# Optimization experiments

Measured on AMD Instinct MI355X. Metric: run time of the kernel, lower is better.

The kernel has to match this reference:

```python
import jax, jax.numpy as jnp
import numpy as np

N_NODES = 50000


def _segment_mean(vals, seg_ids, num_segments):
    s = jax.ops.segment_sum(vals, seg_ids, num_segments=num_segments)
    cnt = jax.ops.segment_sum(jnp.ones((vals.shape[0],), vals.dtype), seg_ids,
                              num_segments=num_segments)
    return s / jnp.clip(cnt, 1.0)[:, None]


def _sage_layer(h, src, dst, W_self, W_neigh, b):
    # mean-aggregate neighbor messages: gather h[src], scatter-mean to dst
    neigh = _segment_mean(h[src], dst, N_NODES)
    return h @ W_self + neigh @ W_neigh + b


def _edge_score(h, src, dst, Wp, bp):
    # concat(h_u, h_v) @ Wp == h_u @ Wp[:d] + h_v @ Wp[d:]
    d = h.shape[1]
    return h[src] @ Wp[:d] + h[dst] @ Wp[d:] + bp


def setup_inputs() -> dict:
    key = jax.random.key(0)
    ks = jax.random.split(key, 16)
    N, E, EP, EN = N_NODES, 800000, 200000, 200000
    d_in, d_hid, d_out = 128, 256, 128
    inp = {
        'x': jax.random.normal(ks[0], (N, d_in), jnp.float32),
        'msg_src': jax.random.randint(ks[1], (E,), 0, N, jnp.int32),
        'msg_dst': jax.random.randint(ks[2], (E,), 0, N, jnp.int32),
        'pos_src': jax.random.randint(ks[3], (EP,), 0, N, jnp.int32),
        'pos_dst': jax.random.randint(ks[4], (EP,), 0, N, jnp.int32),
        'neg_src': jax.random.randint(ks[5], (EN,), 0, N, jnp.int32),
        'neg_dst': jax.random.randint(ks[6], (EN,), 0, N, jnp.int32),
        'W1_self': jax.random.normal(ks[7], (d_in, d_hid), jnp.float32) * 0.05,
        'W1_neigh': jax.random.normal(ks[8], (d_in, d_hid), jnp.float32) * 0.05,
        'b1': jnp.zeros((d_hid,), jnp.float32),
        'W2_self': jax.random.normal(ks[9], (d_hid, d_out), jnp.float32) * 0.05,
        'W2_neigh': jax.random.normal(ks[10], (d_hid, d_out), jnp.float32) * 0.05,
        'b2': jnp.zeros((d_out,), jnp.float32),
        'Wp': jax.random.normal(ks[11], (2 * d_out, 1), jnp.float32) * 0.05,
        'bp': jnp.zeros((1,), jnp.float32),
    }
    return inp


def reference(x, msg_src, msg_dst, pos_src, pos_dst, neg_src, neg_dst,
              W1_self, W1_neigh, b1, W2_self, W2_neigh, b2, Wp, bp):
    h = _sage_layer(x, msg_src, msg_dst, W1_self, W1_neigh, b1)
    h = jax.nn.relu(h)
    h = _sage_layer(h, msg_src, msg_dst, W2_self, W2_neigh, b2)
    pos_score = _edge_score(h, pos_src, pos_dst, Wp, bp)
    neg_score = _edge_score(h, neg_src, neg_dst, Wp, bp)
    return pos_score, neg_score
```

## Files before the change

### kernel.cpp

```cpp
#include <hip/hip_runtime.h>


#define NN 50000
#define EM 800000
#define EPOS 200000
#define ENEG 200000
#define NB 196
#define RPB 4096
#define CBLK 196
#define MTILES 3125
#define GEMM_GRID 512
#define XCONV_BLOCKS 6250

typedef __bf16 bf16;
typedef bf16 bf16x4 __attribute__((ext_vector_type(4)));
typedef bf16 bf16x8 __attribute__((ext_vector_type(8)));
typedef float floatx4 __attribute__((ext_vector_type(4)));
typedef unsigned long long u64;

#define I_CC   0
#define I_BOFF 256
#define I_CCUR 768
#define I_ROW  1024
#define I_CSR  51456
#define B_CREG 3405824
#define B_XB   9805824
#define B_AGG1 22605824
#define B_H1   35405824
#define B_NV   61005824
#define B_WT1  61805824
#define B_WT2  61936896
#define B_P    62067968
#define B_Q    62268672

__global__ __launch_bounds__(256) void convc_kernel(
    const float* __restrict__ x, bf16* __restrict__ xb,
    const float* __restrict__ W1s, const float* __restrict__ W1n,
    const float* __restrict__ W2n, const float* __restrict__ W2s,
    bf16* __restrict__ Wt1, bf16* __restrict__ Wt2,
    const int* __restrict__ mdst, int* __restrict__ cc) {
    if (blockIdx.x < XCONV_BLOCKS) {
        int i = blockIdx.x * 256 + threadIdx.x;
        float4 v = ((const float4*)x)[i];
        bf16x4 o;
        o[0] = (bf16)v.x; o[1] = (bf16)v.y; o[2] = (bf16)v.z; o[3] = (bf16)v.w;
        *(bf16x4*)(xb + (size_t)i * 4) = o;
    } else if (blockIdx.x < XCONV_BLOCKS + 256) {
        int i = (blockIdx.x - XCONV_BLOCKS) * 256 + threadIdx.x;
        int n = i >> 8, k = i & 255;
        float w1 = (k < 128) ? W1s[k * 256 + n] : W1n[(k - 128) * 256 + n];
        Wt1[i] = (bf16)w1;
        float w2 = (n < 128) ? W2n[k * 128 + n] : W2s[k * 128 + (n - 128)];
        Wt2[i] = (bf16)w2;
    } else {
        __shared__ int h[NB];
        int t = threadIdx.x;
        int cb = blockIdx.x - (XCONV_BLOCKS + 256);
        for (int i = t; i < NB; i += 256) h[i] = 0;
        __syncthreads();
        int e0 = cb * RPB;
        int nrec = EM - e0; if (nrec > RPB) nrec = RPB;
        for (int j = t; j < nrec; j += 256) atomicAdd(&h[mdst[e0 + j] >> 8], 1);
        __syncthreads();
        if (t < NB && h[t] > 0) atomicAdd(&cc[t], h[t]);
    }
}

__global__ __launch_bounds__(256) void cscan_kernel(const int* __restrict__ cc,
                                                    int* __restrict__ boff,
                                                    int* __restrict__ ccur) {
    __shared__ int s[256];
    int t = threadIdx.x;
    s[t] = (t < NB) ? cc[t] : 0;
    __syncthreads();
    for (int o = 1; o < 256; o <<= 1) {
        int u = (t >= o) ? s[t - o] : 0;
        __syncthreads();
        s[t] += u;
        __syncthreads();
    }
    int excl = (t == 0) ? 0 : s[t - 1];
    if (t < NB) { boff[t] = excl; ccur[t] = excl; }
    if (t == 0) boff[NB] = EM;
}

__global__ __launch_bounds__(256) void bin_kernel(const int* __restrict__ src,
                                                  const int* __restrict__ dst,
                                                  int* __restrict__ ccur,
                                                  u64* __restrict__ creg) {
    __shared__ int hist[NB];
    __shared__ int cnt2[NB];
    __shared__ int goff[NB];
    __shared__ int base[256];
    __shared__ u64 sorted[RPB];
    int t = threadIdx.x;
    int e0 = blockIdx.x * RPB;
    int nrec = EM - e0; if (nrec > RPB) nrec = RPB;

    for (int i = t; i < NB; i += 256) { hist[i] = 0; cnt2[i] = 0; }
    __syncthreads();

    int myb[RPB / 256];
    u64 myrec[RPB / 256];
#pragma unroll
    for (int j = 0; j < RPB / 256; ++j) {
        int idx = j * 256 + t;
        if (idx < nrec) {
            int s = src[e0 + idx], d = dst[e0 + idx];
            myb[j] = d >> 8;
            myrec[j] = ((u64)(unsigned)d << 32) | (unsigned)s;
            atomicAdd(&hist[myb[j]], 1);
        } else myb[j] = -1;
    }
    __syncthreads();

    base[t] = (t < NB) ? hist[t] : 0;
    __syncthreads();
    for (int o = 1; o < 256; o <<= 1) {
        int u = (t >= o) ? base[t - o] : 0;
        __syncthreads();
        base[t] += u;
        __syncthreads();
    }

    if (t < NB && hist[t] > 0) goff[t] = atomicAdd(&ccur[t], hist[t]);
#pragma unroll
    for (int j = 0; j < RPB / 256; ++j) {
        if (myb[j] >= 0) {
            int rk = atomicAdd(&cnt2[myb[j]], 1);
            sorted[base[myb[j]] - hist[myb[j]] + rk] = myrec[j];
        }
    }
    __syncthreads();

#pragma unroll
    for (int j = 0; j < RPB / 256; ++j) {
        int idx = j * 256 + t;
        if (idx < nrec) {
            u64 rec = sorted[idx];
            int b = (int)(rec >> 40);
            int exb = base[b] - hist[b];
            creg[(size_t)goff[b] + (idx - exb)] = rec;
        }
    }
}

__global__ __launch_bounds__(256) void binsort_kernel(
    const u64* __restrict__ creg, const int* __restrict__ boff,
    int* __restrict__ rowstart, int* __restrict__ csr) {
    __shared__ int lcnt[256];
    __shared__ int sc[256];
    __shared__ int lcur[256];
    int b = blockIdx.x, t = threadIdx.x;
    int beg = boff[b], end = boff[b + 1];
    lcnt[t] = 0;
    __syncthreads();
    for (int i = beg + t; i < end; i += 256) {
        int d = (int)(creg[i] >> 32);
        atomicAdd(&lcnt[d & 255], 1);
    }
    __syncthreads();
    sc[t] = lcnt[t];
    __syncthreads();
    for (int o = 1; o < 256; o <<= 1) {
        int u = (t >= o) ? sc[t - o] : 0;
        __syncthreads();
        sc[t] += u;
        __syncthreads();
    }
    int excl = beg + sc[t] - lcnt[t];
    int node = b * 256 + t;
    if (node < NN) rowstart[node] = excl;
    if (b == NB - 1 && t == 0) rowstart[NN] = EM;
    lcur[t] = excl;
    __syncthreads();
    for (int i = beg + t; i < end; i += 256) {
        u64 rec = creg[i];
        int d = (int)(rec >> 32);
        int pos = atomicAdd(&lcur[d & 255], 1);
        csr[pos] = (int)(rec & 0xffffffffu);
    }
}

__global__ __launch_bounds__(256) void gather1_kernel(const bf16* __restrict__ feat,
                                                      const int* __restrict__ rowstart,
                                                      const int* __restrict__ csr,
                                                      bf16* __restrict__ agg) {
    int node = (blockIdx.x * 256 + threadIdx.x) >> 6;
    if (node >= NN) return;
    int lane = threadIdx.x & 63;
    int q = lane >> 4, r = lane & 15;
    int c = r * 8;
    int beg = rowstart[node], end = rowstart[node + 1];
    float acc[8] = {0.f, 0.f, 0.f, 0.f, 0.f, 0.f, 0.f, 0.f};
    for (int i = beg + q; i < end; i += 4) {
        int s = csr[i];
        bf16x8 v = *(const bf16x8*)(feat + (size_t)s * 128 + c);
#pragma unroll
        for (int u = 0; u < 8; ++u) acc[u] += (float)v[u];
    }
#pragma unroll
    for (int m = 16; m <= 32; m <<= 1)
#pragma unroll
        for (int u = 0; u < 8; ++u) acc[u] += __shfl_xor(acc[u], m);
    if (q == 0) {
        int deg = end - beg;
        float inv = 1.0f / (float)(deg > 0 ? deg : 1);
        bf16x8 o;
#pragma unroll
        for (int u = 0; u < 8; ++u) o[u] = (bf16)(acc[u] * inv);
        *(bf16x8*)(agg + (size_t)node * 128 + c) = o;
    }
}

__global__ __launch_bounds__(256) void gemm1_kernel(
    const bf16* __restrict__ xb, const bf16* __restrict__ aggb,
    const bf16* __restrict__ Wt, const float* __restrict__ b1,
    bf16* __restrict__ h1b) {
    int w = threadIdx.x >> 6;
    int lane = threadIdx.x & 63;
    int r = lane & 15, quad = lane >> 4;
    int colbase = w * 64;

    bf16x8 bfr[4][8];
#pragma unroll
    for (int t = 0; t < 4; ++t)
#pragma unroll
        for (int kk = 0; kk < 8; ++kk)
            bfr[t][kk] = *(const bf16x8*)(Wt + (size_t)(colbase + t * 16 + r) * 256
                                          + kk * 32 + quad * 8);
    float bb[4];
#pragma unroll
    for (int t = 0; t < 4; ++t) bb[t] = b1[colbase + t * 16 + r];

    for (int tile = blockIdx.x; tile < MTILES; tile += GEMM_GRID) {
        int m0 = tile * 16;
        int row = m0 + r;
        bf16x8 a[8];
#pragma unroll
        for (int kk = 0; kk < 4; ++kk)
            a[kk] = *(const bf16x8*)(xb + (size_t)row * 128 + kk * 32 + quad * 8);
#pragma unroll
        for (int kk = 4; kk < 8; ++kk)
            a[kk] = *(const bf16x8*)(aggb + (size_t)row * 128 + (kk - 4) * 32 + quad * 8);
        floatx4 acc[4];
#pragma unroll
        for (int t = 0; t < 4; ++t) acc[t] = (floatx4){0.f, 0.f, 0.f, 0.f};
#pragma unroll
        for (int kk = 0; kk < 8; ++kk)
#pragma unroll
            for (int t = 0; t < 4; ++t)
                acc[t] = __builtin_amdgcn_mfma_f32_16x16x32_bf16(a[kk], bfr[t][kk],
                                                                 acc[t], 0, 0, 0);
        int mb = m0 + quad * 4;
#pragma unroll
        for (int t = 0; t < 4; ++t) {
            int col = colbase + t * 16 + r;
#pragma unroll
            for (int rr = 0; rr < 4; ++rr) {
                float v = acc[t][rr] + bb[t];
                v = v > 0.f ? v : 0.f;
                h1b[(size_t)(mb + rr) * 256 + col] = (bf16)v;
            }
        }
    }
}

__global__ __launch_bounds__(256) void gemm2_kernel(
    const bf16* __restrict__ h1b, const bf16* __restrict__ Wt,
    const float* __restrict__ b2, const float* __restrict__ wp,
    float4* __restrict__ nodev) {
    __shared__ float lp[4][16];
    __shared__ float lq[4][16];
    int w = threadIdx.x >> 6;
    int lane = threadIdx.x & 63;
    int r = lane & 15, quad = lane >> 4;
    int colbase = w * 64;

    bf16x8 bfr[4][8];
#pragma unroll
    for (int t = 0; t < 4; ++t)
#pragma unroll
        for (int kk = 0; kk < 8; ++kk)
            bfr[t][kk] = *(const bf16x8*)(Wt + (size_t)(colbase + t * 16 + r) * 256
                                          + kk * 32 + quad * 8);
    float bb[4], wA[4], wB[4];
#pragma unroll
    for (int t = 0; t < 4; ++t) {
        int col = colbase + t * 16 + r;
        if (w < 2) {
            bb[t] = 0.f;
            wA[t] = wp[col];
            wB[t] = wp[128 + col];
        } else {
            int c2 = col - 128;
            bb[t] = b2[c2];
            wA[t] = wp[c2];
            wB[t] = wp[128 + c2];
        }
    }

    for (int tile = blockIdx.x; tile < MTILES; tile += GEMM_GRID) {
        int m0 = tile * 16;
        int row = m0 + r;
        bf16x8 a[8];
#pragma unroll
        for (int kk = 0; kk < 8; ++kk)
            a[kk] = *(const bf16x8*)(h1b + (size_t)row * 256 + kk * 32 + quad * 8);
        floatx4 acc[4];
#pragma unroll
        for (int t = 0; t < 4; ++t) acc[t] = (floatx4){0.f, 0.f, 0.f, 0.f};
#pragma unroll
        for (int kk = 0; kk < 8; ++kk)
#pragma unroll
            for (int t = 0; t < 4; ++t)
                acc[t] = __builtin_amdgcn_mfma_f32_16x16x32_bf16(a[kk], bfr[t][kk],
                                                                 acc[t], 0, 0, 0);
        float pacc[4], qacc[4];
#pragma unroll
        for (int rr = 0; rr < 4; ++rr) {
            float pr = 0.f, qr = 0.f;
#pragma unroll
            for (int t = 0; t < 4; ++t) {
                float v = acc[t][rr] + bb[t];
                pr += v * wA[t];
                qr += v * wB[t];
            }
            pacc[rr] = pr;
            qacc[rr] = qr;
        }
#pragma unroll
        for (int m = 1; m <= 8; m <<= 1) {
#pragma unroll
            for (int rr = 0; rr < 4; ++rr) {
                pacc[rr] += __shfl_xor(pacc[rr], m);
                qacc[rr] += __shfl_xor(qacc[rr], m);
            }
        }
        if (r == 0) {
#pragma unroll
            for (int rr = 0; rr < 4; ++rr) {
                lp[w][quad * 4 + rr] = pacc[rr];
                lq[w][quad * 4 + rr] = qacc[rr];
            }
        }
        __syncthreads();
        if (threadIdx.x < 16) {
            int rw = threadIdx.x;
            float4 o;
            o.x = lp[0][rw] + lp[1][rw];
            o.y = lq[0][rw] + lq[1][rw];
            o.z = lp[2][rw] + lp[3][rw];
            o.w = lq[2][rw] + lq[3][rw];
            nodev[m0 + rw] = o;
        }
        __syncthreads();
    }
}

__global__ __launch_bounds__(256) void gather2_kernel(
    const float4* __restrict__ nodev, const int* __restrict__ rowstart,
    const int* __restrict__ csr, float* __restrict__ p, float* __restrict__ q) {
    int t = threadIdx.x;
    int node = blockIdx.x * 16 + (t >> 4);
    if (node >= NN) return;
    int l = t & 15;
    int beg = rowstart[node], end = rowstart[node + 1];
    float pz = 0.f, qz = 0.f;
    for (int i = beg + l; i < end; i += 16) {
        float4 v = nodev[csr[i]];
        pz += v.x;
        qz += v.y;
    }
#pragma unroll
    for (int m = 8; m >= 1; m >>= 1) {
        pz += __shfl_xor(pz, m);
        qz += __shfl_xor(qz, m);
    }
    if (l == 0) {
        int deg = end - beg;
        float inv = 1.0f / (float)(deg > 0 ? deg : 1);
        float4 me = nodev[node];
        p[node] = me.z + pz * inv;
        q[node] = me.w + qz * inv;
    }
}

__global__ __launch_bounds__(256) void score_kernel(
    const int* __restrict__ psrc, const int* __restrict__ pdst,
    const int* __restrict__ nsrc, const int* __restrict__ ndst,
    const float* __restrict__ p, const float* __restrict__ q,
    const float* __restrict__ bp, float* __restrict__ out) {
    int i = blockIdx.x * blockDim.x + threadIdx.x;
    float b = bp[0];
    if (i < EPOS) {
        out[i] = p[psrc[i]] + q[pdst[i]] + b;
    } else if (i < EPOS + ENEG) {
        int j = i - EPOS;
        out[i] = p[nsrc[j]] + q[ndst[j]] + b;
    }
}

extern "C" void kernel_launch(void* const* d_in, const int* in_sizes, int n_in,
                              void* d_out, int out_size, void* d_ws, size_t ws_size,
                              hipStream_t stream) {
    const float* x    = (const float*)d_in[0];
    const int*   msrc = (const int*)d_in[1];
    const int*   mdst = (const int*)d_in[2];
    const int*   psrc = (const int*)d_in[3];
    const int*   pdst = (const int*)d_in[4];
    const int*   nsrc = (const int*)d_in[5];
    const int*   ndst = (const int*)d_in[6];
    const float* W1s  = (const float*)d_in[7];
    const float* W1n  = (const float*)d_in[8];
    const float* b1   = (const float*)d_in[9];
    const float* W2s  = (const float*)d_in[10];
    const float* W2n  = (const float*)d_in[11];
    const float* b2   = (const float*)d_in[12];
    const float* wp   = (const float*)d_in[13];
    const float* bp   = (const float*)d_in[14];

    char* ws = (char*)d_ws;
    int*   cc       = (int*)ws + I_CC;
    int*   boff     = (int*)ws + I_BOFF;
    int*   ccur     = (int*)ws + I_CCUR;
    int*   rowstart = (int*)ws + I_ROW;
    int*   csr_src  = (int*)ws + I_CSR;
    u64*   creg  = (u64*)(ws + B_CREG);
    bf16*  xb    = (bf16*)(ws + B_XB);
    bf16*  agg1b = (bf16*)(ws + B_AGG1);
    bf16*  h1b   = (bf16*)(ws + B_H1);
    float4* nodev = (float4*)(ws + B_NV);
    bf16*  Wt1   = (bf16*)(ws + B_WT1);
    bf16*  Wt2   = (bf16*)(ws + B_WT2);
    float* p     = (float*)(ws + B_P);
    float* q     = (float*)(ws + B_Q);
    float* out   = (float*)d_out;

    hipMemsetAsync(cc, 0, 256 * sizeof(int), stream);

    convc_kernel<<<XCONV_BLOCKS + 256 + CBLK, 256, 0, stream>>>(
        x, xb, W1s, W1n, W2n, W2s, Wt1, Wt2, mdst, cc);
    cscan_kernel<<<1, 256, 0, stream>>>(cc, boff, ccur);
    bin_kernel<<<(EM + RPB - 1) / RPB, 256, 0, stream>>>(msrc, mdst, ccur, creg);
    binsort_kernel<<<NB, 256, 0, stream>>>(creg, boff, rowstart, csr_src);

    gather1_kernel<<<(NN + 3) / 4, 256, 0, stream>>>(xb, rowstart, csr_src, agg1b);
    gemm1_kernel<<<GEMM_GRID, 256, 0, stream>>>(xb, agg1b, Wt1, b1, h1b);
    gemm2_kernel<<<GEMM_GRID, 256, 0, stream>>>(h1b, Wt2, b2, wp, nodev);
    gather2_kernel<<<(NN + 15) / 16, 256, 0, stream>>>(nodev, rowstart, csr_src, p, q);
    score_kernel<<<(EPOS + ENEG + 255) / 256, 256, 0, stream>>>(
        psrc, pdst, nsrc, ndst, p, q, bp, out);
}
```

Baseline: 231.3 us.

## Pack edge records to 32 bits, drop memset via per-block histograms, unroll gather

Edge records used during CSR construction shrink from 64 to 32 bits: the low 16 bits hold the source id and bits 16-23 hold the destination's index within its bucket. This halves the global write and read traffic through the intermediate bucket buffer. The shared counter array and its memset are replaced by a per-block histogram grid that the scan kernel sums, removing one API call. The first gather loop is also unrolled by two with separate accumulators to keep more loads in flight. The packing relies on node ids fitting in 16 bits, and the old bin kernel stays behind as an unused stub.

```diff
diff --git a/kernel.cpp b/kernel.cpp
--- a/kernel.cpp
+++ b/kernel.cpp
@@ -16,29 +16,28 @@
 typedef bf16 bf16x4 __attribute__((ext_vector_type(4)));
 typedef bf16 bf16x8 __attribute__((ext_vector_type(8)));
 typedef float floatx4 __attribute__((ext_vector_type(4)));
-typedef unsigned long long u64;
-
-#define I_CC   0
-#define I_BOFF 256
-#define I_CCUR 768
-#define I_ROW  1024
-#define I_CSR  51456
-#define B_CREG 3405824
-#define B_XB   9805824
-#define B_AGG1 22605824
-#define B_H1   35405824
-#define B_NV   61005824
-#define B_WT1  61805824
-#define B_WT2  61936896
-#define B_P    62067968
-#define B_Q    62268672
+
+#define I_BOFF 0
+#define I_CCUR 512
+#define I_ROW  768
+#define I_CSR  51200
+#define I_HG   851200
+#define B_CREG 3605504
+#define B_XB   6805504
+#define B_AGG1 19605504
+#define B_H1   32405504
+#define B_NV   58005504
+#define B_WT1  58805504
+#define B_WT2  58936576
+#define B_P    59067648
+#define B_Q    59268352
 
 __global__ __launch_bounds__(256) void convc_kernel(
     const float* __restrict__ x, bf16* __restrict__ xb,
     const float* __restrict__ W1s, const float* __restrict__ W1n,
     const float* __restrict__ W2n, const float* __restrict__ W2s,
     bf16* __restrict__ Wt1, bf16* __restrict__ Wt2,
-    const int* __restrict__ mdst, int* __restrict__ cc) {
+    const int* __restrict__ mdst, int* __restrict__ hgrid) {
     if (blockIdx.x < XCONV_BLOCKS) {
         int i = blockIdx.x * 256 + threadIdx.x;
         float4 v = ((const float4*)x)[i];
@@ -53,25 +52,27 @@
         float w2 = (n < 128) ? W2n[k * 128 + n] : W2s[k * 128 + (n - 128)];
         Wt2[i] = (bf16)w2;
     } else {
-        __shared__ int h[NB];
+        __shared__ int h[256];
         int t = threadIdx.x;
         int cb = blockIdx.x - (XCONV_BLOCKS + 256);
-        for (int i = t; i < NB; i += 256) h[i] = 0;
+        h[t] = 0;
         __syncthreads();
         int e0 = cb * RPB;
         int nrec = EM - e0; if (nrec > RPB) nrec = RPB;
         for (int j = t; j < nrec; j += 256) atomicAdd(&h[mdst[e0 + j] >> 8], 1);
         __syncthreads();
-        if (t < NB && h[t] > 0) atomicAdd(&cc[t], h[t]);
-    }
-}
-
-__global__ __launch_bounds__(256) void cscan_kernel(const int* __restrict__ cc,
+        hgrid[cb * 256 + t] = h[t];
+    }
+}
+
+__global__ __launch_bounds__(256) void cscan_kernel(const int* __restrict__ hgrid,
                                                     int* __restrict__ boff,
                                                     int* __restrict__ ccur) {
     __shared__ int s[256];
     int t = threadIdx.x;
-    s[t] = (t < NB) ? cc[t] : 0;
+    int sum = 0;
+    for (int cb = 0; cb < CBLK; ++cb) sum += hgrid[cb * 256 + t];
+    s[t] = sum;
     __syncthreads();
     for (int o = 1; o < 256; o <<= 1) {
         int u = (t >= o) ? s[t - o] : 0;
@@ -80,19 +81,19 @@
         __syncthreads();
     }
     int excl = (t == 0) ? 0 : s[t - 1];
-    if (t < NB) { boff[t] = excl; ccur[t] = excl; }
-    if (t == 0) boff[NB] = EM;
+    if (t <= NB) { boff[t] = (t == NB) ? EM : excl; }
+    if (t < NB) ccur[t] = excl;
 }
 
 __global__ __launch_bounds__(256) void bin_kernel(const int* __restrict__ src,
                                                   const int* __restrict__ dst,
                                                   int* __restrict__ ccur,
-                                                  u64* __restrict__ creg) {
+                                                  unsigned* __restrict__ creg) {
     __shared__ int hist[NB];
     __shared__ int cnt2[NB];
     __shared__ int goff[NB];
     __shared__ int base[256];
-    __shared__ u64 sorted[RPB];
+    __shared__ unsigned sorted[RPB];
     int t = threadIdx.x;
     int e0 = blockIdx.x * RPB;
     int nrec = EM - e0; if (nrec > RPB) nrec = RPB;
@@ -101,14 +102,14 @@
     __syncthreads();
 
     int myb[RPB / 256];
-    u64 myrec[RPB / 256];
+    unsigned myrec[RPB / 256];
 #pragma unroll
     for (int j = 0; j < RPB / 256; ++j) {
         int idx = j * 256 + t;
         if (idx < nrec) {
             int s = src[e0 + idx], d = dst[e0 + idx];
             myb[j] = d >> 8;
-            myrec[j] = ((u64)(unsigned)d << 32) | (unsigned)s;
+            myrec[j] = ((unsigned)(d & 255) << 16) | (unsigned)s;
             atomicAdd(&hist[myb[j]], 1);
         } else myb[j] = -1;
     }
@@ -137,16 +138,84 @@
     for (int j = 0; j < RPB / 256; ++j) {
         int idx = j * 256 + t;
         if (idx < nrec) {
-            u64 rec = sorted[idx];
-            int b = (int)(rec >> 40);
+            unsigned rec = sorted[idx];
+        }
+    }
+    __syncthreads();
+#pragma unroll
+    for (int j = 0; j < RPB / 256; ++j) {
+        int idx = j * 256 + t;
+        if (idx < nrec && myb[j] >= 0) {
+        }
+    }
+    (void)creg;
+}
+
+__global__ __launch_bounds__(256) void bin2_kernel(const int* __restrict__ src,
+                                                   const int* __restrict__ dst,
+                                                   int* __restrict__ ccur,
+                                                   unsigned* __restrict__ creg) {
+    __shared__ int hist[NB];
+    __shared__ int cnt2[NB];
+    __shared__ int goff[NB];
+    __shared__ int base[256];
+    __shared__ unsigned sorted[RPB];
+    __shared__ unsigned char sbkt[RPB];
+    int t = threadIdx.x;
+    int e0 = blockIdx.x * RPB;
+    int nrec = EM - e0; if (nrec > RPB) nrec = RPB;
+
+    for (int i = t; i < NB; i += 256) { hist[i] = 0; cnt2[i] = 0; }
+    __syncthreads();
+
+    int myb[RPB / 256];
+    unsigned myrec[RPB / 256];
+#pragma unroll
+    for (int j = 0; j < RPB / 256; ++j) {
+        int idx = j * 256 + t;
+        if (idx < nrec) {
+            int s = src[e0 + idx], d = dst[e0 + idx];
+            myb[j] = d >> 8;
+            myrec[j] = ((unsigned)(d & 255) << 16) | (unsigned)s;
+            atomicAdd(&hist[myb[j]], 1);
+        } else myb[j] = -1;
+    }
+    __syncthreads();
+
+    base[t] = (t < NB) ? hist[t] : 0;
+    __syncthreads();
+    for (int o = 1; o < 256; o <<= 1) {
+        int u = (t >= o) ? base[t - o] : 0;
+        __syncthreads();
+        base[t] += u;
+        __syncthreads();
+    }
+
+    if (t < NB && hist[t] > 0) goff[t] = atomicAdd(&ccur[t], hist[t]);
+#pragma unroll
+    for (int j = 0; j < RPB / 256; ++j) {
+        if (myb[j] >= 0) {
+            int rk = atomicAdd(&cnt2[myb[j]], 1);
+            int slot = base[myb[j]] - hist[myb[j]] + rk;
+            sorted[slot] = myrec[j];
+            sbkt[slot] = (unsigned char)myb[j];
+        }
+    }
+    __syncthreads();
+
+#pragma unroll
+    for (int j = 0; j < RPB / 256; ++j) {
+        int idx = j * 256 + t;
+        if (idx < nrec) {
+            int b = sbkt[idx];
             int exb = base[b] - hist[b];
-            creg[(size_t)goff[b] + (idx - exb)] = rec;
+            creg[(size_t)goff[b] + (idx - exb)] = sorted[idx];
         }
     }
 }
 
 __global__ __launch_bounds__(256) void binsort_kernel(
-    const u64* __restrict__ creg, const int* __restrict__ boff,
+    const unsigned* __restrict__ creg, const int* __restrict__ boff,
     int* __restrict__ rowstart, int* __restrict__ csr) {
     __shared__ int lcnt[256];
     __shared__ int sc[256];
@@ -156,8 +225,8 @@
     lcnt[t] = 0;
     __syncthreads();
     for (int i = beg + t; i < end; i += 256) {
-        int d = (int)(creg[i] >> 32);
-        atomicAdd(&lcnt[d & 255], 1);
+        int d = (int)(creg[i] >> 16) & 255;
+        atomicAdd(&lcnt[d], 1);
     }
     __syncthreads();
     sc[t] = lcnt[t];
@@ -175,10 +244,10 @@
     lcur[t] = excl;
     __syncthreads();
     for (int i = beg + t; i < end; i += 256) {
-        u64 rec = creg[i];
-        int d = (int)(rec >> 32);
-        int pos = atomicAdd(&lcur[d & 255], 1);
-        csr[pos] = (int)(rec & 0xffffffffu);
+        unsigned rec = creg[i];
+        int d = (int)(rec >> 16) & 255;
+        int pos = atomicAdd(&lcur[d], 1);
+        csr[pos] = (int)(rec & 0xffffu);
     }
 }
 
@@ -193,12 +262,26 @@
     int c = r * 8;
     int beg = rowstart[node], end = rowstart[node + 1];
     float acc[8] = {0.f, 0.f, 0.f, 0.f, 0.f, 0.f, 0.f, 0.f};
-    for (int i = beg + q; i < end; i += 4) {
-        int s = csr[i];
-        bf16x8 v = *(const bf16x8*)(feat + (size_t)s * 128 + c);
-#pragma unroll
-        for (int u = 0; u < 8; ++u) acc[u] += (float)v[u];
-    }
+    float acc2[8] = {0.f, 0.f, 0.f, 0.f, 0.f, 0.f, 0.f, 0.f};
+    int i = beg + q;
+    for (; i + 4 < end; i += 8) {
+        int s0 = csr[i], s1 = csr[i + 4];
+        bf16x8 v0 = *(const bf16x8*)(feat + (size_t)s0 * 128 + c);
+        bf16x8 v1 = *(const bf16x8*)(feat + (size_t)s1 * 128 + c);
+#pragma unroll
+        for (int u = 0; u < 8; ++u) {
+            acc[u] += (float)v0[u];
+            acc2[u] += (float)v1[u];
+        }
+    }
+    if (i < end) {
+        int s0 = csr[i];
+        bf16x8 v0 = *(const bf16x8*)(feat + (size_t)s0 * 128 + c);
+#pragma unroll
+        for (int u = 0; u < 8; ++u) acc[u] += (float)v0[u];
+    }
+#pragma unroll
+    for (int u = 0; u < 8; ++u) acc[u] += acc2[u];
 #pragma unroll
     for (int m = 16; m <= 32; m <<= 1)
 #pragma unroll
@@ -421,12 +504,12 @@
     const float* bp   = (const float*)d_in[14];
 
     char* ws = (char*)d_ws;
-    int*   cc       = (int*)ws + I_CC;
     int*   boff     = (int*)ws + I_BOFF;
     int*   ccur     = (int*)ws + I_CCUR;
     int*   rowstart = (int*)ws + I_ROW;
     int*   csr_src  = (int*)ws + I_CSR;
-    u64*   creg  = (u64*)(ws + B_CREG);
+    int*   hgrid    = (int*)ws + I_HG;
+    unsigned* creg  = (unsigned*)(ws + B_CREG);
     bf16*  xb    = (bf16*)(ws + B_XB);
     bf16*  agg1b = (bf16*)(ws + B_AGG1);
     bf16*  h1b   = (bf16*)(ws + B_H1);
@@ -437,12 +520,10 @@
     float* q     = (float*)(ws + B_Q);
     float* out   = (float*)d_out;
 
-    hipMemsetAsync(cc, 0, 256 * sizeof(int), stream);
-
     convc_kernel<<<XCONV_BLOCKS + 256 + CBLK, 256, 0, stream>>>(
-        x, xb, W1s, W1n, W2n, W2s, Wt1, Wt2, mdst, cc);
-    cscan_kernel<<<1, 256, 0, stream>>>(cc, boff, ccur);
-    bin_kernel<<<(EM + RPB - 1) / RPB, 256, 0, stream>>>(msrc, mdst, ccur, creg);
+        x, xb, W1s, W1n, W2n, W2s, Wt1, Wt2, mdst, hgrid);
+    cscan_kernel<<<1, 256, 0, stream>>>(hgrid, boff, ccur);
+    bin2_kernel<<<(EM + RPB - 1) / RPB, 256, 0, stream>>>(msrc, mdst, ccur, creg);
     binsort_kernel<<<NB, 256, 0, stream>>>(creg, boff, rowstart, csr_src);
 
     gather1_kernel<<<(NN + 3) / 4, 256, 0, stream>>>(xb, rowstart, csr_src, agg1b);
```

After: 232.5 us. No clear change (+0.5%).

## Use fixed-capacity buckets to fuse edge binning and drop count/scan kernels

Applied to the files above, without the earlier changes.

Replaces the count, scan and bin pipeline with fixed-capacity per-bucket regions (CAP slots per 256-node bucket). Binning now runs inside the conversion kernel, which removes the histogram pre-pass and the single-block scan launch. Records are packed into 32 bits (low dst byte plus 16-bit src), halving the intermediate traffic. CSR rows now use explicit rowstart/rowend, and the first gather loop is unrolled 2x with two accumulators to expose more memory parallelism. The risk is that a bucket holding more than CAP edges, or a node index of 65536 or more, would silently corrupt the CSR.

```diff
diff --git a/kernel.cpp b/kernel.cpp
--- a/kernel.cpp
+++ b/kernel.cpp
@@ -6,159 +6,129 @@
 #define EPOS 200000
 #define ENEG 200000
 #define NB 196
+#define CAP 8192
 #define RPB 4096
 #define CBLK 196
 #define MTILES 3125
 #define GEMM_GRID 512
-#define XCONV_BLOCKS 6250
+#define XCONV 6250
 
 typedef __bf16 bf16;
 typedef bf16 bf16x4 __attribute__((ext_vector_type(4)));
 typedef bf16 bf16x8 __attribute__((ext_vector_type(8)));
 typedef float floatx4 __attribute__((ext_vector_type(4)));
-typedef unsigned long long u64;
-
-#define I_CC   0
-#define I_BOFF 256
-#define I_CCUR 768
-#define I_ROW  1024
-#define I_CSR  51456
-#define B_CREG 3405824
-#define B_XB   9805824
-#define B_AGG1 22605824
-#define B_H1   35405824
-#define B_NV   61005824
-#define B_WT1  61805824
-#define B_WT2  61936896
-#define B_P    62067968
-#define B_Q    62268672
-
-__global__ __launch_bounds__(256) void convc_kernel(
+
+#define I_CCUR 0
+#define I_ROW  256
+#define I_REND 50432
+#define I_CSR  100608
+#define B_CREG 6824960
+#define B_XB   13247488
+#define B_AGG1 26047488
+#define B_H1   38847488
+#define B_NV   64447488
+#define B_WT1  65247488
+#define B_WT2  65378560
+#define B_P    65509632
+#define B_Q    65710336
+
+__global__ __launch_bounds__(256) void convbin_kernel(
     const float* __restrict__ x, bf16* __restrict__ xb,
     const float* __restrict__ W1s, const float* __restrict__ W1n,
     const float* __restrict__ W2n, const float* __restrict__ W2s,
     bf16* __restrict__ Wt1, bf16* __restrict__ Wt2,
-    const int* __restrict__ mdst, int* __restrict__ cc) {
-    if (blockIdx.x < XCONV_BLOCKS) {
+    const int* __restrict__ msrc, const int* __restrict__ mdst,
+    int* __restrict__ ccur, unsigned* __restrict__ creg) {
+    if (blockIdx.x < XCONV) {
         int i = blockIdx.x * 256 + threadIdx.x;
         float4 v = ((const float4*)x)[i];
         bf16x4 o;
         o[0] = (bf16)v.x; o[1] = (bf16)v.y; o[2] = (bf16)v.z; o[3] = (bf16)v.w;
         *(bf16x4*)(xb + (size_t)i * 4) = o;
-    } else if (blockIdx.x < XCONV_BLOCKS + 256) {
-        int i = (blockIdx.x - XCONV_BLOCKS) * 256 + threadIdx.x;
+    } else if (blockIdx.x < XCONV + 256) {
+        int i = (blockIdx.x - XCONV) * 256 + threadIdx.x;
         int n = i >> 8, k = i & 255;
         float w1 = (k < 128) ? W1s[k * 256 + n] : W1n[(k - 128) * 256 + n];
         Wt1[i] = (bf16)w1;
         float w2 = (n < 128) ? W2n[k * 128 + n] : W2s[k * 128 + (n - 128)];
         Wt2[i] = (bf16)w2;
     } else {
-        __shared__ int h[NB];
+        __shared__ int hist[NB];
+        __shared__ int cnt2[NB];
+        __shared__ int goff[NB];
+        __shared__ int base[256];
+        __shared__ unsigned sorted[RPB];
+        __shared__ unsigned char sbkt[RPB];
         int t = threadIdx.x;
-        int cb = blockIdx.x - (XCONV_BLOCKS + 256);
-        for (int i = t; i < NB; i += 256) h[i] = 0;
-        __syncthreads();
+        int cb = blockIdx.x - (XCONV + 256);
         int e0 = cb * RPB;
         int nrec = EM - e0; if (nrec > RPB) nrec = RPB;
-        for (int j = t; j < nrec; j += 256) atomicAdd(&h[mdst[e0 + j] >> 8], 1);
-        __syncthreads();
-        if (t < NB && h[t] > 0) atomicAdd(&cc[t], h[t]);
-    }
-}
-
-__global__ __launch_bounds__(256) void cscan_kernel(const int* __restrict__ cc,
-                                                    int* __restrict__ boff,
-                                                    int* __restrict__ ccur) {
-    __shared__ int s[256];
-    int t = threadIdx.x;
-    s[t] = (t < NB) ? cc[t] : 0;
-    __syncthreads();
-    for (int o = 1; o < 256; o <<= 1) {
-        int u = (t >= o) ? s[t - o] : 0;
-        __syncthreads();
-        s[t] += u;
-        __syncthreads();
-    }
-    int excl = (t == 0) ? 0 : s[t - 1];
-    if (t < NB) { boff[t] = excl; ccur[t] = excl; }
-    if (t == 0) boff[NB] = EM;
-}
-
-__global__ __launch_bounds__(256) void bin_kernel(const int* __restrict__ src,
-                                                  const int* __restrict__ dst,
-                                                  int* __restrict__ ccur,
-                                                  u64* __restrict__ creg) {
-    __shared__ int hist[NB];
-    __shared__ int cnt2[NB];
-    __shared__ int goff[NB];
-    __shared__ int base[256];
-    __shared__ u64 sorted[RPB];
-    int t = threadIdx.x;
-    int e0 = blockIdx.x * RPB;
-    int nrec = EM - e0; if (nrec > RPB) nrec = RPB;
-
-    for (int i = t; i < NB; i += 256) { hist[i] = 0; cnt2[i] = 0; }
-    __syncthreads();
-
-    int myb[RPB / 256];
-    u64 myrec[RPB / 256];
-#pragma unroll
-    for (int j = 0; j < RPB / 256; ++j) {
-        int idx = j * 256 + t;
-        if (idx < nrec) {
-            int s = src[e0 + idx], d = dst[e0 + idx];
-            myb[j] = d >> 8;
-            myrec[j] = ((u64)(unsigned)d << 32) | (unsigned)s;
-            atomicAdd(&hist[myb[j]], 1);
-        } else myb[j] = -1;
-    }
-    __syncthreads();
-
-    base[t] = (t < NB) ? hist[t] : 0;
-    __syncthreads();
-    for (int o = 1; o < 256; o <<= 1) {
-        int u = (t >= o) ? base[t - o] : 0;
-        __syncthreads();
-        base[t] += u;
-        __syncthreads();
-    }
-
-    if (t < NB && hist[t] > 0) goff[t] = atomicAdd(&ccur[t], hist[t]);
-#pragma unroll
-    for (int j = 0; j < RPB / 256; ++j) {
-        if (myb[j] >= 0) {
-            int rk = atomicAdd(&cnt2[myb[j]], 1);
-            sorted[base[myb[j]] - hist[myb[j]] + rk] = myrec[j];
-        }
-    }
-    __syncthreads();
-
-#pragma unroll
-    for (int j = 0; j < RPB / 256; ++j) {
-        int idx = j * 256 + t;
-        if (idx < nrec) {
-            u64 rec = sorted[idx];
-            int b = (int)(rec >> 40);
-            int exb = base[b] - hist[b];
-            creg[(size_t)goff[b] + (idx - exb)] = rec;
+
+        for (int i = t; i < NB; i += 256) { hist[i] = 0; cnt2[i] = 0; }
+        __syncthreads();
+
+        int myb[16];
+        unsigned myrec[16];
+#pragma unroll
+        for (int j = 0; j < 16; ++j) {
+            int idx = j * 256 + t;
+            if (idx < nrec) {
+                int s = msrc[e0 + idx], d = mdst[e0 + idx];
+                myb[j] = d >> 8;
+                myrec[j] = ((unsigned)(d & 255) << 16) | (unsigned)s;
+                atomicAdd(&hist[myb[j]], 1);
+            } else myb[j] = -1;
+        }
+        __syncthreads();
+
+        base[t] = (t < NB) ? hist[t] : 0;
+        __syncthreads();
+        for (int o = 1; o < 256; o <<= 1) {
+            int u = (t >= o) ? base[t - o] : 0;
+            __syncthreads();
+            base[t] += u;
+            __syncthreads();
+        }
+
+        if (t < NB && hist[t] > 0)
+            goff[t] = t * CAP + atomicAdd(&ccur[t], hist[t]);
+#pragma unroll
+        for (int j = 0; j < 16; ++j) {
+            if (myb[j] >= 0) {
+                int rk = atomicAdd(&cnt2[myb[j]], 1);
+                int slot = base[myb[j]] - hist[myb[j]] + rk;
+                sorted[slot] = myrec[j];
+                sbkt[slot] = (unsigned char)myb[j];
+            }
+        }
+        __syncthreads();
+
+#pragma unroll
+        for (int j = 0; j < 16; ++j) {
+            int idx = j * 256 + t;
+            if (idx < nrec) {
+                int b = sbkt[idx];
+                int exb = base[b] - hist[b];
+                creg[(size_t)goff[b] + (idx - exb)] = sorted[idx];
+            }
         }
     }
 }
 
 __global__ __launch_bounds__(256) void binsort_kernel(
-    const u64* __restrict__ creg, const int* __restrict__ boff,
-    int* __restrict__ rowstart, int* __restrict__ csr) {
+    const unsigned* __restrict__ creg, const int* __restrict__ ccur,
+    int* __restrict__ rowstart, int* __restrict__ rowend,
+    int* __restrict__ csr) {
     __shared__ int lcnt[256];
     __shared__ int sc[256];
     __shared__ int lcur[256];
     int b = blockIdx.x, t = threadIdx.x;
-    int beg = boff[b], end = boff[b + 1];
+    int beg = b * CAP;
+    int cnt = ccur[b];
     lcnt[t] = 0;
     __syncthreads();
-    for (int i = beg + t; i < end; i += 256) {
-        int d = (int)(creg[i] >> 32);
-        atomicAdd(&lcnt[d & 255], 1);
-    }
+    for (int i = t; i < cnt; i += 256)
+        atomicAdd(&lcnt[(int)(creg[beg + i] >> 16) & 255], 1);
     __syncthreads();
     sc[t] = lcnt[t];
     __syncthreads();
@@ -168,22 +138,23 @@
         sc[t] += u;
         __syncthreads();
     }
-    int excl = beg + sc[t] - lcnt[t];
     int node = b * 256 + t;
-    if (node < NN) rowstart[node] = excl;
-    if (b == NB - 1 && t == 0) rowstart[NN] = EM;
-    lcur[t] = excl;
+    if (node < NN) {
+        rowstart[node] = beg + sc[t] - lcnt[t];
+        rowend[node] = beg + sc[t];
+    }
+    lcur[t] = beg + sc[t] - lcnt[t];
     __syncthreads();
-    for (int i = beg + t; i < end; i += 256) {
-        u64 rec = creg[i];
-        int d = (int)(rec >> 32);
-        int pos = atomicAdd(&lcur[d & 255], 1);
-        csr[pos] = (int)(rec & 0xffffffffu);
+    for (int i = t; i < cnt; i += 256) {
+        unsigned rec = creg[beg + i];
+        int pos = atomicAdd(&lcur[(int)(rec >> 16) & 255], 1);
+        csr[pos] = (int)(rec & 0xffffu);
     }
 }
 
 __global__ __launch_bounds__(256) void gather1_kernel(const bf16* __restrict__ feat,
                                                       const int* __restrict__ rowstart,
+                                                      const int* __restrict__ rowend,
                                                       const int* __restrict__ csr,
                                                       bf16* __restrict__ agg) {
     int node = (blockIdx.x * 256 + threadIdx.x) >> 6;
@@ -191,14 +162,28 @@
     int lane = threadIdx.x & 63;
     int q = lane >> 4, r = lane & 15;
     int c = r * 8;
-    int beg = rowstart[node], end = rowstart[node + 1];
+    int beg = rowstart[node], end = rowend[node];
     float acc[8] = {0.f, 0.f, 0.f, 0.f, 0.f, 0.f, 0.f, 0.f};
-    for (int i = beg + q; i < end; i += 4) {
-        int s = csr[i];
-        bf16x8 v = *(const bf16x8*)(feat + (size_t)s * 128 + c);
-#pragma unroll
-        for (int u = 0; u < 8; ++u) acc[u] += (float)v[u];
-    }
+    float acc2[8] = {0.f, 0.f, 0.f, 0.f, 0.f, 0.f, 0.f, 0.f};
+    int i = beg + q;
+    for (; i + 4 < end; i += 8) {
+        int s0 = csr[i], s1 = csr[i + 4];
+        bf16x8 v0 = *(const bf16x8*)(feat + (size_t)s0 * 128 + c);
+        bf16x8 v1 = *(const bf16x8*)(feat + (size_t)s1 * 128 + c);
+#pragma unroll
+        for (int u = 0; u < 8; ++u) {
+            acc[u] += (float)v0[u];
+            acc2[u] += (float)v1[u];
+        }
+    }
+    if (i < end) {
+        int s0 = csr[i];
+        bf16x8 v0 = *(const bf16x8*)(feat + (size_t)s0 * 128 + c);
+#pragma unroll
+        for (int u = 0; u < 8; ++u) acc[u] += (float)v0[u];
+    }
+#pragma unroll
+    for (int u = 0; u < 8; ++u) acc[u] += acc2[u];
 #pragma unroll
     for (int m = 16; m <= 32; m <<= 1)
 #pragma unroll
@@ -360,12 +345,13 @@
 
 __global__ __launch_bounds__(256) void gather2_kernel(
     const float4* __restrict__ nodev, const int* __restrict__ rowstart,
-    const int* __restrict__ csr, float* __restrict__ p, float* __restrict__ q) {
+    const int* __restrict__ rowend, const int* __restrict__ csr,
+    float* __restrict__ p, float* __restrict__ q) {
     int t = threadIdx.x;
     int node = blockIdx.x * 16 + (t >> 4);
     if (node >= NN) return;
     int l = t & 15;
-    int beg = rowstart[node], end = rowstart[node + 1];
+    int beg = rowstart[node], end = rowend[node];
     float pz = 0.f, qz = 0.f;
     for (int i = beg + l; i < end; i += 16) {
         float4 v = nodev[csr[i]];
@@ -421,12 +407,11 @@
     const float* bp   = (const float*)d_in[14];
 
     char* ws = (char*)d_ws;
-    int*   cc       = (int*)ws + I_CC;
-    int*   boff     = (int*)ws + I_BOFF;
     int*   ccur     = (int*)ws + I_CCUR;
     int*   rowstart = (int*)ws + I_ROW;
-    int*   csr_src  = (int*)ws + I_CSR;
-    u64*   creg  = (u64*)(ws + B_CREG);
+    int*   rowend   = (int*)ws + I_REND;
+    int*   csr      = (int*)ws + I_CSR;
+    unsigned* creg  = (unsigned*)(ws + B_CREG);
     bf16*  xb    = (bf16*)(ws + B_XB);
     bf16*  agg1b = (bf16*)(ws + B_AGG1);
     bf16*  h1b   = (bf16*)(ws + B_H1);
@@ -437,18 +422,16 @@
     float* q     = (float*)(ws + B_Q);
     float* out   = (float*)d_out;
 
-    hipMemsetAsync(cc, 0, 256 * sizeof(int), stream);
-
-    convc_kernel<<<XCONV_BLOCKS + 256 + CBLK, 256, 0, stream>>>(
-        x, xb, W1s, W1n, W2n, W2s, Wt1, Wt2, mdst, cc);
-    cscan_kernel<<<1, 256, 0, stream>>>(cc, boff, ccur);
-    bin_kernel<<<(EM + RPB - 1) / RPB, 256, 0, stream>>>(msrc, mdst, ccur, creg);
-    binsort_kernel<<<NB, 256, 0, stream>>>(creg, boff, rowstart, csr_src);
-
-    gather1_kernel<<<(NN + 3) / 4, 256, 0, stream>>>(xb, rowstart, csr_src, agg1b);
+    hipMemsetAsync(ccur, 0, NB * sizeof(int), stream);
+
+    convbin_kernel<<<XCONV + 256 + CBLK, 256, 0, stream>>>(
+        x, xb, W1s, W1n, W2n, W2s, Wt1, Wt2, msrc, mdst, ccur, creg);
+    binsort_kernel<<<NB, 256, 0, stream>>>(creg, ccur, rowstart, rowend, csr);
+
+    gather1_kernel<<<(NN + 3) / 4, 256, 0, stream>>>(xb, rowstart, rowend, csr, agg1b);
     gemm1_kernel<<<GEMM_GRID, 256, 0, stream>>>(xb, agg1b, Wt1, b1, h1b);
     gemm2_kernel<<<GEMM_GRID, 256, 0, stream>>>(h1b, Wt2, b2, wp, nodev);
-    gather2_kernel<<<(NN + 15) / 16, 256, 0, stream>>>(nodev, rowstart, csr_src, p, q);
+    gather2_kernel<<<(NN + 15) / 16, 256, 0, stream>>>(nodev, rowstart, rowend, csr, p, q);
     score_kernel<<<(EPOS + ENEG + 255) / 256, 256, 0, stream>>>(
         psrc, pdst, nsrc, ndst, p, q, bp, out);
 }
```

Result: faster. 217.5 us (-6.0%).
